# Kernel optimization log

Hardware: AMD Instinct MI355X
Metric: run time of the kernel (lower is better)

The kernel has to match this reference:

```python
import jax, jax.numpy as jnp
import numpy as np

B, N, D = 32, 1024, 2
M0, R = 0.05, 2


def setup_inputs() -> dict:
    key = jax.random.key(0)
    k1, k2, k3 = jax.random.split(key, 3)
    inp = jax.random.normal(k1, (B, N, D), dtype=jnp.float32)
    weight = jax.random.uniform(k2, (B, N), dtype=jnp.float32)
    grid = jax.random.normal(k3, (N, D), dtype=jnp.float32)
    return {"input": inp, "weight": weight, "grid": grid}


def _pairwise_dist(x, g):
    # x: [B,N,D], g: [N,D] -> euclidean distance [B,N,N] via gram trick
    x2 = jnp.sum(x * x, -1)[:, :, None]          # [B,N,1]
    g2 = jnp.sum(g * g, -1)[None, None, :]       # [1,1,N]
    d2 = x2 + g2 - 2.0 * jnp.einsum('bnd,md->bnm', x, g)
    return jnp.sqrt(jnp.maximum(d2, 0.0))


def _dtm(knn_dist, knn_index, weight, wb, r):
    # knn_dist/knn_index: [B,N,k]; weight: [B,N]; wb: [B,1,1]
    knn_w = jnp.take_along_axis(weight[:, None, :], knn_index, axis=-1)  # [B,N,k]
    cum_w = jnp.cumsum(knn_w, -1)
    # searchsorted(left) == count of strictly-smaller prefix sums
    k_idx = jnp.sum(cum_w < wb, -1, keepdims=True)          # [B,N,1]
    k_idx = jnp.minimum(k_idx, knn_dist.shape[-1] - 1)
    if r == 2:
        r_dist = jnp.square(knn_dist)
    elif r == 1:
        r_dist = knn_dist
    else:
        r_dist = knn_dist ** r
    cum_d = jnp.cumsum(r_dist * knn_w, -1)
    val = jnp.take_along_axis(cum_d + r_dist * (wb - cum_w), k_idx, axis=-1)
    val = val / wb
    if r == 2:
        val = jnp.sqrt(val)
    elif r != 1:
        val = val ** (1.0 / r)
    return val[..., 0]  # [B,N]


def reference(input, weight, grid):
    # weight_bound = m0 * total mass per batch
    wb = M0 * jnp.sum(weight, -1, keepdims=True)            # [B,1]
    # data-dependent k (torch does this in no_grad with .item())
    sw_cum = jnp.cumsum(jnp.sort(weight, -1), -1)
    idx = jnp.sum(sw_cum < wb, -1)                          # searchsorted left, per batch
    max_k = min(int(jnp.max(idx)) + 1, N)
    # brute-force KNN (r=2 euclidean)
    dist = _pairwise_dist(input, grid)                      # [B,N,N]
    neg_top, knn_index = jax.lax.top_k(-dist, max_k)        # smallest k distances
    knn_dist = -neg_top
    return _dtm(knn_dist, knn_index, weight, wb[:, :, None], R)
```

## Files before the change

kernel.cpp:

```cpp
#include <hip/hip_runtime.h>
#include <math.h>


constexpr int   N_GRID   = 1024;
constexpr int   PER_LANE = 16;
constexpr float M0_      = 0.05f;

template<int CTRL, int RM>
__device__ __forceinline__ float dpp_fadd(float v) {
    int moved = __builtin_amdgcn_update_dpp(0, __float_as_int(v), CTRL, RM, 0xF, true);
    return v + __int_as_float(moved);
}
template<int CTRL, int RM>
__device__ __forceinline__ float dpp_fmax(float v) {
    int moved = __builtin_amdgcn_update_dpp(0, __float_as_int(v), CTRL, RM, 0xF, true);
    return fmaxf(v, __int_as_float(moved));
}

__device__ __forceinline__ float wave_sum_u(float v) {
    v = dpp_fadd<0x111, 0xF>(v);
    v = dpp_fadd<0x112, 0xF>(v);
    v = dpp_fadd<0x114, 0xF>(v);
    v = dpp_fadd<0x118, 0xF>(v);
    v = dpp_fadd<0x142, 0xA>(v);
    v = dpp_fadd<0x143, 0xC>(v);
    return __uint_as_float((unsigned)__builtin_amdgcn_readlane(__float_as_int(v), 63));
}
__device__ __forceinline__ float wave_max_u(float v) {
    v = dpp_fmax<0x111, 0xF>(v);
    v = dpp_fmax<0x112, 0xF>(v);
    v = dpp_fmax<0x114, 0xF>(v);
    v = dpp_fmax<0x118, 0xF>(v);
    v = dpp_fmax<0x142, 0xA>(v);
    v = dpp_fmax<0x143, 0xC>(v);
    return __uint_as_float((unsigned)__builtin_amdgcn_readlane(__float_as_int(v), 63));
}

__global__ __launch_bounds__(256) void dtm_kernel(
    const float* __restrict__ input,
    const float* __restrict__ weight,
    const float* __restrict__ grid,
    float* __restrict__ out)
{
    const int wave = threadIdx.x >> 6;
    const int lane = threadIdx.x & 63;
    const int q    = (blockIdx.x << 2) + wave;
    const int b    = q >> 10;

    const float2 xq = reinterpret_cast<const float2*>(input)[q];

    const int base = lane * PER_LANE;
    const float4* w4 = reinterpret_cast<const float4*>(weight + b * N_GRID + base);
    const float4* g4 = reinterpret_cast<const float4*>(grid + 2 * base);

    float4 wv[4], gv[8];
    #pragma unroll
    for (int i = 0; i < 4; ++i) wv[i] = w4[i];
    #pragma unroll
    for (int i = 0; i < 8; ++i) gv[i] = g4[i];

    float d2[PER_LANE], w[PER_LANE];
    float wsum = 0.f, mx = 0.f;
    #pragma unroll
    for (int i = 0; i < 8; ++i) {
        float dx0 = xq.x - gv[i].x, dy0 = xq.y - gv[i].y;
        float dx1 = xq.x - gv[i].z, dy1 = xq.y - gv[i].w;
        d2[2*i]   = dx0 * dx0 + dy0 * dy0;
        d2[2*i+1] = dx1 * dx1 + dy1 * dy1;
        mx = fmaxf(mx, fmaxf(d2[2*i], d2[2*i+1]));
    }
    #pragma unroll
    for (int i = 0; i < 4; ++i) {
        w[4*i+0] = wv[i].x; w[4*i+1] = wv[i].y;
        w[4*i+2] = wv[i].z; w[4*i+3] = wv[i].w;
        wsum += wv[i].x + wv[i].y + wv[i].z + wv[i].w;
    }
    const float total = wave_sum_u(wsum);
    const float wb    = M0_ * total;
    mx = wave_max_u(mx);

    float lo = 0.f, Wlo = 0.f;
    float hi = mx,  Whi = total;
    int side = 0;
    #pragma unroll 1
    for (int it = 0; it < 16; ++it) {
        if ((hi - lo) * (Whi - wb) <= 2e-3f * wb * hi + 1e-12f) break;
        if (hi - lo <= 1e-4f * hi) break;
        float frac = (wb - Wlo) / (Whi - Wlo);
        frac = fminf(fmaxf(frac, 0.04f), 0.96f);
        const float t = lo + (hi - lo) * frac;
        float sv = 0.f;
        #pragma unroll
        for (int k = 0; k < PER_LANE; ++k)
            sv += (d2[k] <= t) ? w[k] : 0.f;
        const float s = wave_sum_u(sv);
        if (s >= wb) {
            if (side == 1) Wlo = wb - 0.5f * (wb - Wlo);
            hi = t; Whi = s; side = 1;
        } else {
            if (side == -1) Whi = wb + 0.5f * (Whi - wb);
            lo = t; Wlo = s; side = -1;
        }
    }
    const float t = hi;

    float Av = 0.f, Sv = 0.f;
    #pragma unroll
    for (int k = 0; k < PER_LANE; ++k) {
        const bool in = (d2[k] < t);
        Av += in ? d2[k] * w[k] : 0.f;
        Sv += in ? w[k] : 0.f;
    }
    const float A = wave_sum_u(Av);
    const float S = wave_sum_u(Sv);

    if (lane == 0) out[q] = sqrtf(fmaxf((A + t * (wb - S)) / wb, 0.f));
}

extern "C" void kernel_launch(void* const* d_in, const int* in_sizes, int n_in,
                              void* d_out, int out_size, void* d_ws, size_t ws_size,
                              hipStream_t stream) {
    const float* input  = (const float*)d_in[0];
    const float* weight = (const float*)d_in[1];
    const float* grid   = (const float*)d_in[2];
    float* out = (float*)d_out;

    const int total_q = 32 * 1024;
    dim3 blk(256);
    dim3 grd(total_q / 4);
    hipLaunchKernelGGL(dtm_kernel, grd, blk, 0, stream,
                       input, weight, grid, out);
}
```

Before: 46.02 us.

## Replace single-pivot threshold search with three-pivot search per pass

```diff
diff --git a/kernel.cpp b/kernel.cpp
--- a/kernel.cpp
+++ b/kernel.cpp
@@ -16,27 +16,33 @@
     int moved = __builtin_amdgcn_update_dpp(0, __float_as_int(v), CTRL, RM, 0xF, true);
     return fmaxf(v, __int_as_float(moved));
 }
-
-__device__ __forceinline__ float wave_sum_u(float v) {
-    v = dpp_fadd<0x111, 0xF>(v);
-    v = dpp_fadd<0x112, 0xF>(v);
-    v = dpp_fadd<0x114, 0xF>(v);
-    v = dpp_fadd<0x118, 0xF>(v);
-    v = dpp_fadd<0x142, 0xA>(v);
-    v = dpp_fadd<0x143, 0xC>(v);
-    return __uint_as_float((unsigned)__builtin_amdgcn_readlane(__float_as_int(v), 63));
-}
-__device__ __forceinline__ float wave_max_u(float v) {
-    v = dpp_fmax<0x111, 0xF>(v);
-    v = dpp_fmax<0x112, 0xF>(v);
-    v = dpp_fmax<0x114, 0xF>(v);
-    v = dpp_fmax<0x118, 0xF>(v);
-    v = dpp_fmax<0x142, 0xA>(v);
-    v = dpp_fmax<0x143, 0xC>(v);
+__device__ __forceinline__ float lane63(float v) {
     return __uint_as_float((unsigned)__builtin_amdgcn_readlane(__float_as_int(v), 63));
 }
 
-__global__ __launch_bounds__(256) void dtm_kernel(
+__device__ __forceinline__ float wave_sum_u(float v) {
+    v = dpp_fadd<0x111,0xF>(v); v = dpp_fadd<0x112,0xF>(v);
+    v = dpp_fadd<0x114,0xF>(v); v = dpp_fadd<0x118,0xF>(v);
+    v = dpp_fadd<0x142,0xA>(v); v = dpp_fadd<0x143,0xC>(v);
+    return lane63(v);
+}
+__device__ __forceinline__ float wave_max_u(float v) {
+    v = dpp_fmax<0x111,0xF>(v); v = dpp_fmax<0x112,0xF>(v);
+    v = dpp_fmax<0x114,0xF>(v); v = dpp_fmax<0x118,0xF>(v);
+    v = dpp_fmax<0x142,0xA>(v); v = dpp_fmax<0x143,0xC>(v);
+    return lane63(v);
+}
+__device__ __forceinline__ void wave_sum3_u(float& a, float& b, float& c) {
+    a = dpp_fadd<0x111,0xF>(a); b = dpp_fadd<0x111,0xF>(b); c = dpp_fadd<0x111,0xF>(c);
+    a = dpp_fadd<0x112,0xF>(a); b = dpp_fadd<0x112,0xF>(b); c = dpp_fadd<0x112,0xF>(c);
+    a = dpp_fadd<0x114,0xF>(a); b = dpp_fadd<0x114,0xF>(b); c = dpp_fadd<0x114,0xF>(c);
+    a = dpp_fadd<0x118,0xF>(a); b = dpp_fadd<0x118,0xF>(b); c = dpp_fadd<0x118,0xF>(c);
+    a = dpp_fadd<0x142,0xA>(a); b = dpp_fadd<0x142,0xA>(b); c = dpp_fadd<0x142,0xA>(c);
+    a = dpp_fadd<0x143,0xC>(a); b = dpp_fadd<0x143,0xC>(b); c = dpp_fadd<0x143,0xC>(c);
+    a = lane63(a); b = lane63(b); c = lane63(c);
+}
+
+__global__ __launch_bounds__(256, 4) void dtm_kernel(
     const float* __restrict__ input,
     const float* __restrict__ weight,
     const float* __restrict__ grid,
@@ -75,32 +81,46 @@
         w[4*i+2] = wv[i].z; w[4*i+3] = wv[i].w;
         wsum += wv[i].x + wv[i].y + wv[i].z + wv[i].w;
     }
+
     const float total = wave_sum_u(wsum);
     const float wb    = M0_ * total;
     mx = wave_max_u(mx);
 
     float lo = 0.f, Wlo = 0.f;
     float hi = mx,  Whi = total;
-    int side = 0;
     #pragma unroll 1
-    for (int it = 0; it < 16; ++it) {
+    for (int pass = 0; pass < 8; ++pass) {
         if ((hi - lo) * (Whi - wb) <= 2e-3f * wb * hi + 1e-12f) break;
         if (hi - lo <= 1e-4f * hi) break;
-        float frac = (wb - Wlo) / (Whi - Wlo);
-        frac = fminf(fmaxf(frac, 0.04f), 0.96f);
-        const float t = lo + (hi - lo) * frac;
-        float sv = 0.f;
+
+        float f1, f2, f3;
+        if (pass < 3) {
+            const float fr = (wb - Wlo) / (Whi - Wlo);
+            f2 = fminf(fmaxf(fr, 0.03f), 0.95f);
+            f1 = 0.5f * f2;
+            f3 = fminf(2.0f * f2, 0.5f * (1.0f + f2));
+        } else {
+            f1 = 0.25f; f2 = 0.5f; f3 = 0.75f;
+        }
+        const float width = hi - lo;
+        const float t1 = lo + width * f1;
+        const float t2 = lo + width * f2;
+        const float t3 = lo + width * f3;
+
+        float c1 = 0.f, c2 = 0.f, c3 = 0.f;
         #pragma unroll
-        for (int k = 0; k < PER_LANE; ++k)
-            sv += (d2[k] <= t) ? w[k] : 0.f;
-        const float s = wave_sum_u(sv);
-        if (s >= wb) {
-            if (side == 1) Wlo = wb - 0.5f * (wb - Wlo);
-            hi = t; Whi = s; side = 1;
-        } else {
-            if (side == -1) Whi = wb + 0.5f * (Whi - wb);
-            lo = t; Wlo = s; side = -1;
+        for (int k = 0; k < PER_LANE; ++k) {
+            const float dk = d2[k], wk = w[k];
+            c1 += (dk <= t1) ? wk : 0.f;
+            c2 += (dk <= t2) ? wk : 0.f;
+            c3 += (dk <= t3) ? wk : 0.f;
         }
+        wave_sum3_u(c1, c2, c3);
+
+        if (c1 >= wb)      { hi = t1; Whi = c1; }
+        else if (c2 >= wb) { lo = t1; Wlo = c1; hi = t2; Whi = c2; }
+        else if (c3 >= wb) { lo = t2; Wlo = c2; hi = t3; Whi = c3; }
+        else               { lo = t3; Wlo = c3; }
     }
     const float t = hi;
 
```

Result: slower. 53.55 us (+16.4%).
